# Optimization experiments

Hardware: AMD Instinct MI355X
Metric: run time of the kernel (lower is better)

The kernel has to match this reference:

```python
import jax, jax.numpy as jnp
import numpy as np

ANCESTOR_INDEX = [[], [0], [0], [0], [0, 1], [0, 2], [0, 3], [0, 1, 4], [0, 2, 5], [0, 3, 6], [0, 1, 4, 7], [0, 2, 5, 8], [0, 3, 6, 9], [0, 3, 6, 9], [0, 3, 6, 9], [0, 3, 6, 9, 12], [0, 3, 6, 9, 13], [0, 3, 6, 9, 14], [0, 3, 6, 9, 13, 16], [0, 3, 6, 9, 14, 17], [0, 3, 6, 9, 13, 16, 18], [0, 3, 6, 9, 14, 17, 19], [0, 3, 6, 9, 13, 16, 18, 20], [0, 3, 6, 9, 14, 17, 19, 21]]
HID = 1024
NP6 = 6
MAXIN = HID + NP6 * 8 + 6


def setup_inputs() -> dict:
    key = jax.random.key(0)
    ks = jax.random.split(key, 18)
    B, T = 2048, 16
    s = 0.02
    inp = {
        'x': jax.random.normal(ks[0], (B, T, 256), jnp.float32),
        'init_pose': jax.random.normal(ks[1], (B, T, 144), jnp.float32) * 0.1,
        'init_shape': jax.random.normal(ks[2], (B, T, 10), jnp.float32) * 0.1,
        'init_cam': jax.random.normal(ks[3], (B, T, 3), jnp.float32) * 0.1,
        'fc1_w': jax.random.normal(ks[4], (HID, 256 + 10), jnp.float32) * s,
        'fc1_b': jnp.zeros((HID,), jnp.float32),
        'fc2_w': jax.random.normal(ks[5], (HID, 256 + 144), jnp.float32) * s,
        'fc2_b': jnp.zeros((HID,), jnp.float32),
        'decshape_w': jax.random.normal(ks[6], (10, HID), jnp.float32) * s,
        'decshape_b': jnp.zeros((10,), jnp.float32),
        'deccam_w': jax.random.normal(ks[7], (3, 2 * HID + 3), jnp.float32) * s,
        'deccam_b': jnp.zeros((3,), jnp.float32),
        'ktd_w': jax.random.normal(ks[8], (24, NP6, MAXIN), jnp.float32) * 0.01,
        'ktd_b': jnp.zeros((24, NP6), jnp.float32),
    }
    return inp


def reference(x, init_pose, init_shape, init_cam, fc1_w, fc1_b, fc2_w, fc2_b,
              decshape_w, decshape_b, deccam_w, deccam_b, ktd_w, ktd_b):
    # fc1 / fc2 (dropout is identity in eval mode)
    xc_shape_cam = jnp.concatenate([x, init_shape], -1) @ fc1_w.T + fc1_b   # [B,T,HID]
    xc_pose_cam = jnp.concatenate([x, init_pose], -1) @ fc2_w.T + fc2_b     # [B,T,HID]

    pose = []
    for j, anc in enumerate(ANCESTOR_INDEX):
        parts = [xc_pose_cam] + [pose[i] for i in anc] + [init_pose[..., j:j + 6]]
        inp = jnp.concatenate(parts, -1)
        pad = MAXIN - inp.shape[-1]
        if pad:
            inp = jnp.pad(inp, ((0, 0), (0, 0), (0, pad)))
        pose.append(jnp.einsum('btd,od->bto', inp, ktd_w[j]) + ktd_b[j])
    pred_pose = jnp.concatenate(pose, -1) + init_pose                        # [B,T,144]

    pred_shape = xc_shape_cam @ decshape_w.T + decshape_b + init_shape      # [B,T,10]
    pred_cam = (jnp.concatenate([xc_pose_cam, xc_shape_cam, init_cam], -1)
                @ deccam_w.T + deccam_b + init_cam)                          # [B,T,3]

    pred_pose = pred_pose.reshape(-1, 144)
    pred_shape = pred_shape.reshape(-1, 10)
    pred_cam = pred_cam.reshape(-1, 3)
    # theta layout matches original output: [cam | pose | shape]
    return jnp.concatenate([pred_cam, pred_pose, pred_shape], -1)           # [B*T,157]
```

## Files before the change

kernel.cpp:

```cpp
#include <hip/hip_runtime.h>
#include <hip/hip_bf16.h>

typedef __attribute__((ext_vector_type(8))) short bf16x8;
typedef __attribute__((ext_vector_type(4))) float f32x4;

static constexpr int ALEN[24] = {0,1,1,1,2,2,2,3,3,3,4,4,4,4,4,5,5,5,6,6,7,7,8,8};
static constexpr int AOFF[24] = {0,0,1,2,3,5,7,9,12,15,18,22,26,30,34,38,43,48,53,59,65,72,79,87};
static constexpr int AFLAT[95] = {
  0, 0, 0,
  0,1, 0,2, 0,3,
  0,1,4, 0,2,5, 0,3,6,
  0,1,4,7, 0,2,5,8, 0,3,6,9, 0,3,6,9, 0,3,6,9,
  0,3,6,9,12, 0,3,6,9,13, 0,3,6,9,14,
  0,3,6,9,13,16, 0,3,6,9,14,17,
  0,3,6,9,13,16,18, 0,3,6,9,14,17,19,
  0,3,6,9,13,16,18,20, 0,3,6,9,14,17,19,21};
static constexpr int LVLN[9] = {1,3,3,3,5,3,2,2,2};
static constexpr int LVLJ[9][5] = {
  {0,0,0,0,0},{1,2,3,0,0},{4,5,6,0,0},{7,8,9,0,0},{10,11,12,13,14},
  {15,16,17,0,0},{18,19,0,0,0},{20,21,0,0,0},{22,23,0,0,0}};

static __device__ __forceinline__ unsigned short f2bf(float f) {
  unsigned int u = __float_as_uint(f);
  u = (u + 0x7fffu + ((u >> 16) & 1u)) >> 16;
  return (unsigned short)u;
}

static __device__ __forceinline__ bf16x8 pack8(float4 lo, float4 hi) {
  bf16x8 r;
  r[0] = (short)f2bf(lo.x); r[1] = (short)f2bf(lo.y);
  r[2] = (short)f2bf(lo.z); r[3] = (short)f2bf(lo.w);
  r[4] = (short)f2bf(hi.x); r[5] = (short)f2bf(hi.y);
  r[6] = (short)f2bf(hi.z); r[7] = (short)f2bf(hi.w);
  return r;
}

__global__ __launch_bounds__(256) void combine_plus(const float* __restrict__ ktd,
                                                    const float* __restrict__ dcw,
                                                    const float* __restrict__ dsw,
                                                    const float* __restrict__ w2,
                                                    const float* __restrict__ b2,
                                                    const float* __restrict__ w1,
                                                    const float* __restrict__ b1,
                                                    float* __restrict__ Gp,
                                                    float* __restrict__ Hp,
                                                    float* __restrict__ S) {
  __shared__ float shpool[5760];
  const int tid = threadIdx.x;

  if (blockIdx.y == 41) {
    if (blockIdx.x >= 4 || blockIdx.z != 0) return;
    float* Sl = shpool;
    const int c0 = blockIdx.x * 36;
    for (int lv = 0; lv < 9; lv++) {
      int units = LVLN[lv] * 54;
      for (int u = tid; u < units; u += 256) {
        int jj = u / 54, rem = u % 54, r = rem / 9, q = rem % 9;
        int j = LVLJ[lv][jj];
        int t = 6 * j + r;
        int cb = c0 + q * 4;
        f32x4 v;
        v[0] = (t == cb)     ? 1.f : 0.f;
        v[1] = (t == cb + 1) ? 1.f : 0.f;
        v[2] = (t == cb + 2) ? 1.f : 0.f;
        v[3] = (t == cb + 3) ? 1.f : 0.f;
        const float* wrow = ktd + (size_t)t * 1078 + 1024;
        for (int a = 0; a < ALEN[j]; a++) {
          int anc = AFLAT[AOFF[j] + a];
          const float* w = wrow + 6 * a;
          #pragma unroll
          for (int k = 0; k < 6; k++) {
            f32x4 s4 = *(const f32x4*)&Sl[(anc * 6 + k) * 40 + q * 4];
            float wk = w[k];
            v[0] += wk * s4[0]; v[1] += wk * s4[1];
            v[2] += wk * s4[2]; v[3] += wk * s4[3];
          }
        }
        *(f32x4*)&Sl[t * 40 + q * 4] = v;
      }
      __syncthreads();
    }
    for (int i = tid; i < 144 * 36; i += 256) {
      int t = i / 36, cc = i % 36;
      S[t * 144 + c0 + cc] = Sl[t * 40 + cc];
    }
    return;
  }

  const bool isH = blockIdx.y >= 37;
  if (isH && blockIdx.x >= 5) return;
  float (*red)[4][64] = (float(*)[4][64])shpool;
  const int w = tid >> 6, lane = tid & 63;
  const int c = blockIdx.x * 64 + lane;
  const int h0 = blockIdx.z * 128 + w * 32;

  const float* vp[4];
  int o0;
  if (!isH) {
    o0 = blockIdx.y * 4;
    #pragma unroll
    for (int oi = 0; oi < 4; oi++) {
      int o = o0 + oi; if (o > 146) o = 146;
      vp[oi] = (o < 144) ? (ktd + (size_t)o * 1078) : (dcw + (size_t)(o - 144) * 2051);
    }
  } else {
    o0 = (blockIdx.y - 37) * 4;
    #pragma unroll
    for (int oi = 0; oi < 4; oi++) {
      int o = o0 + oi; if (o > 12) o = 12;
      vp[oi] = (o < 10) ? (dsw + (size_t)o * 1024) : (dcw + (size_t)(o - 10) * 2051 + 1024);
    }
  }

  float acc[4] = {0.f, 0.f, 0.f, 0.f};
  if (!isH) {
    #pragma unroll 16
    for (int hh = 0; hh < 32; hh++) {
      int h = h0 + hh;
      float wv = (c < 400) ? w2[h * 400 + c] : ((c == 400) ? b2[h] : 0.f);
      #pragma unroll
      for (int oi = 0; oi < 4; oi++) acc[oi] += vp[oi][h] * wv;
    }
  } else {
    #pragma unroll 16
    for (int hh = 0; hh < 32; hh++) {
      int h = h0 + hh;
      float wv = (c < 266) ? w1[h * 266 + c] : ((c == 266) ? b1[h] : 0.f);
      #pragma unroll
      for (int oi = 0; oi < 4; oi++) acc[oi] += vp[oi][h] * wv;
    }
  }

  #pragma unroll
  for (int oi = 0; oi < 4; oi++) red[w][oi][lane] = acc[oi];
  __syncthreads();
  if (w == 0) {
    #pragma unroll
    for (int oi = 0; oi < 4; oi++) {
      int o = o0 + oi;
      float s = red[0][oi][lane] + red[1][oi][lane] + red[2][oi][lane] + red[3][oi][lane];
      if (!isH) {
        if (o < 147 && c <= 400) Gp[(size_t)blockIdx.z * 59200 + o * 401 + c] = s;
      } else {
        if (o < 13 && c <= 266) Hp[(size_t)blockIdx.z * 3520 + o * 267 + c] = s;
      }
    }
  }
}

static __device__ __forceinline__ float gsum(const float* __restrict__ Gp, int t, int c) {
  float s = 0.f;
  #pragma unroll
  for (int z = 0; z < 8; z++) s += Gp[(size_t)z * 59200 + t * 401 + c];
  return s;
}
static __device__ __forceinline__ float hsum(const float* __restrict__ Hp, int t, int c) {
  float s = 0.f;
  #pragma unroll
  for (int z = 0; z < 8; z++) s += Hp[(size_t)z * 3520 + t * 267 + c];
  return s;
}

__global__ __launch_bounds__(256) void assembleM(const float* __restrict__ Gp,
                                                 const float* __restrict__ Hp,
                                                 const float* __restrict__ dcw,
                                                 const float* __restrict__ dcb,
                                                 const float* __restrict__ dsb,
                                                 const float* __restrict__ ktd,
                                                 const float* __restrict__ ktdb,
                                                 float* __restrict__ M0,
                                                 float* __restrict__ C0) {
  int o = blockIdx.x;
  for (int c = threadIdx.x; c < 424; c += 256) {
    float val = 0.f;
    if (c < 413) {
      if (o < 3) {
        if (c < 400) val += gsum(Gp, 144 + o, c);
        if (c < 256) val += hsum(Hp, 10 + o, c);
        if (c >= 400 && c < 410) val += hsum(Hp, 10 + o, 256 + (c - 400));
        if (c >= 410) {
          val += dcw[(size_t)o * 2051 + 2048 + (c - 410)];
          if ((c - 410) == o) val += 1.f;
        }
      } else if (o < 147) {
        int t = o - 3, j = t / 6;
        if (c < 400) val = gsum(Gp, t, c);
        int cj = c - 256 - j;
        if (cj >= 0 && cj < 6) val += ktd[(size_t)t * 1078 + 1024 + 6 * ALEN[j] + cj];
      } else if (o < 157) {
        int s = o - 147;
        if (c < 256) val = hsum(Hp, s, c);
        if (c >= 400 && c < 410) {
          val += hsum(Hp, s, 256 + (c - 400));
          if ((c - 400) == s) val += 1.f;
        }
      }
    }
    M0[o * 424 + c] = val;
  }
  if (threadIdx.x == 0 && o < 157) {
    float bv;
    if (o < 3)        bv = gsum(Gp, 144 + o, 400) + hsum(Hp, 10 + o, 266) + dcb[o];
    else if (o < 147) bv = gsum(Gp, o - 3, 400) + ktdb[o - 3];
    else              bv = hsum(Hp, o - 147, 266) + dsb[o - 147];
    C0[o] = bv;
  }
}

__global__ __launch_bounds__(256) void foldS(const float* __restrict__ S,
                                             const float* __restrict__ M0,
                                             const float* __restrict__ C0,
                                             unsigned short* __restrict__ Mb,
                                             float* __restrict__ Cb) {
  int o = blockIdx.x;
  int c = blockIdx.y * 212 + threadIdx.x;
  bool act = (threadIdx.x < 212) && (c < 424);
  if (o < 3 || o >= 147) {
    if (act) Mb[o * 424 + c] = f2bf(M0[o * 424 + c]);
    if (threadIdx.x == 0 && blockIdx.y == 0) Cb[o] = (o < 157) ? C0[o] : 0.f;
    return;
  }
  int t = o - 3;
  __shared__ float Sl[144];
  if (threadIdx.x < 144) Sl[threadIdx.x] = S[t * 144 + threadIdx.x];
  __syncthreads();
  if (act) {
    float acc = 0.f;
    #pragma unroll 16
    for (int k = 0; k < 144; k++) acc += Sl[k] * M0[(3 + k) * 424 + c];
    if (c == 256 + t) acc += 1.f;
    Mb[o * 424 + c] = f2bf(acc);
  }
  if (threadIdx.x == 0 && blockIdx.y == 0) {
    float acc = 0.f;
    for (int k = 0; k < 144; k++) acc += Sl[k] * C0[3 + k];
    Cb[o] = acc;
  }
}

__global__ __launch_bounds__(512, 4) void main_gemm(const float* __restrict__ x,
                                                    const float* __restrict__ ipose,
                                                    const float* __restrict__ ishape,
                                                    const float* __restrict__ icam,
                                                    const unsigned short* __restrict__ Mb,
                                                    const float* __restrict__ Cb,
                                                    float* __restrict__ out) {
  __shared__ alignas(16) unsigned short Bl[80 * 424];
  const int tid = threadIdx.x;
  const int w = tid >> 6, lane = tid & 63;
  const int m = lane & 15, g = lane >> 4;
  const int h = blockIdx.y;
  const int rowbase = blockIdx.x * 128 + w * 16;
  const int row = rowbase + m;
  const float* xr = x + (size_t)row * 256;
  const float* pr = ipose + (size_t)row * 144;

  {
    const bf16x8* src = (const bf16x8*)(Mb + (size_t)h * 80 * 424);
    bf16x8* dst = (bf16x8*)Bl;
    for (int i = tid; i < 80 * 424 / 8; i += 512) dst[i] = src[i];
  }

  bf16x8 areg[13];
  {
    float4 lo[5], hi[5];
    #pragma unroll
    for (int k = 0; k < 5; k++) {
      const float* p = xr + k * 32 + g * 8;
      lo[k] = *(const float4*)p; hi[k] = *(const float4*)(p + 4);
    }
    #pragma unroll
    for (int k = 0; k < 5; k++) {
      asm volatile("" :: "v"(lo[k].x), "v"(lo[k].y), "v"(lo[k].z), "v"(lo[k].w));
      asm volatile("" :: "v"(hi[k].x), "v"(hi[k].y), "v"(hi[k].z), "v"(hi[k].w));
    }
    #pragma unroll
    for (int k = 0; k < 5; k++) areg[k] = pack8(lo[k], hi[k]);
  }
  {
    float4 lo[4], hi[4];
    #pragma unroll
    for (int k = 0; k < 3; k++) {
      const float* p = xr + (k + 5) * 32 + g * 8;
      lo[k] = *(const float4*)p; hi[k] = *(const float4*)(p + 4);
    }
    {
      const float* p = pr + g * 8;
      lo[3] = *(const float4*)p; hi[3] = *(const float4*)(p + 4);
    }
    #pragma unroll
    for (int k = 0; k < 4; k++) {
      asm volatile("" :: "v"(lo[k].x), "v"(lo[k].y), "v"(lo[k].z), "v"(lo[k].w));
      asm volatile("" :: "v"(hi[k].x), "v"(hi[k].y), "v"(hi[k].z), "v"(hi[k].w));
    }
    #pragma unroll
    for (int k = 0; k < 4; k++) areg[k + 5] = pack8(lo[k], hi[k]);
  }
  {
    float4 lo[4], hi[4];
    #pragma unroll
    for (int k = 0; k < 3; k++) {
      const float* p = pr + (k + 1) * 32 + g * 8;
      lo[k] = *(const float4*)p; hi[k] = *(const float4*)(p + 4);
    }
    if (g < 2) {
      const float* p = pr + 128 + g * 8;
      lo[3] = *(const float4*)p; hi[3] = *(const float4*)(p + 4);
    } else if (g == 2) {
      const float* p = ishape + (size_t)row * 10;
      lo[3] = make_float4(p[0], p[1], p[2], p[3]);
      hi[3] = make_float4(p[4], p[5], p[6], p[7]);
    } else {
      const float* p = ishape + (size_t)row * 10;
      const float* q = icam + (size_t)row * 3;
      lo[3] = make_float4(p[8], p[9], q[0], q[1]);
      hi[3] = make_float4(q[2], 0.f, 0.f, 0.f);
    }
    #pragma unroll
    for (int k = 0; k < 4; k++) {
      asm volatile("" :: "v"(lo[k].x), "v"(lo[k].y), "v"(lo[k].z), "v"(lo[k].w));
      asm volatile("" :: "v"(hi[k].x), "v"(hi[k].y), "v"(hi[k].z), "v"(hi[k].w));
    }
    #pragma unroll
    for (int k = 0; k < 4; k++) areg[k + 9] = pack8(lo[k], hi[k]);
  }

  __syncthreads();

  f32x4 acc[5];
  #pragma unroll
  for (int n = 0; n < 5; n++) acc[n] = (f32x4){0.f, 0.f, 0.f, 0.f};

  #pragma unroll
  for (int k = 0; k < 13; k++) {
    #pragma unroll
    for (int n = 0; n < 5; n++) {
      bf16x8 b = *(const bf16x8*)&Bl[(n * 16 + m) * 424 + k * 32 + g * 8];
      acc[n] = __builtin_amdgcn_mfma_f32_16x16x32_bf16(areg[k], b, acc[n], 0, 0, 0);
    }
  }

  #pragma unroll
  for (int n = 0; n < 5; n++) {
    int col = h * 80 + n * 16 + m;
    if (col < 157) {
      float bias = Cb[col];
      #pragma unroll
      for (int q = 0; q < 4; q++)
        out[(size_t)(rowbase + g * 4 + q) * 157 + col] = acc[n][q] + bias;
    }
  }
}

extern "C" void kernel_launch(void* const* d_in, const int* in_sizes, int n_in,
                              void* d_out, int out_size, void* d_ws, size_t ws_size,
                              hipStream_t stream) {
  const float* x      = (const float*)d_in[0];
  const float* ipose  = (const float*)d_in[1];
  const float* ishape = (const float*)d_in[2];
  const float* icam   = (const float*)d_in[3];
  const float* fc1w   = (const float*)d_in[4];
  const float* fc1b   = (const float*)d_in[5];
  const float* fc2w   = (const float*)d_in[6];
  const float* fc2b   = (const float*)d_in[7];
  const float* dsw    = (const float*)d_in[8];
  const float* dsb    = (const float*)d_in[9];
  const float* dcw    = (const float*)d_in[10];
  const float* dcb    = (const float*)d_in[11];
  const float* ktd    = (const float*)d_in[12];
  const float* ktdb   = (const float*)d_in[13];
  int rows = in_sizes[0] / 256;
  float* ws = (float*)d_ws;

  float* Gp = ws;
  float* Hp = ws + 473600;
  float* M0 = ws + 501760;
  float* C0 = ws + 569600;
  float* S  = ws + 569760;
  float* Cb = ws + 590496;
  unsigned short* Mb = (unsigned short*)(ws + 590656);

  combine_plus<<<dim3(7, 42, 8), 256, 0, stream>>>(ktd, dcw, dsw, fc2w, fc2b,
                                                   fc1w, fc1b, Gp, Hp, S);
  assembleM<<<160, 256, 0, stream>>>(Gp, Hp, dcw, dcb, dsb, ktd, ktdb, M0, C0);
  foldS<<<dim3(160, 2), 256, 0, stream>>>(S, M0, C0, Mb, Cb);
  main_gemm<<<dim3(rows / 128, 2), 512, 0, stream>>>(x, ipose, ishape, icam,
                                                     Mb, Cb, (float*)d_out);
}
```

Measured before the change: 61.85 us.

## Fuse setup kernels into one persistent kernel with software grid barriers

Merges the weight-combine, matrix-assembly and S-fold kernels into a single persistent 256-block kernel that loops over the former work units and separates phases with atomic-counter grid barriers. The aim is to remove kernel launch gaps between the small preprocessing stages. It adds a memset for the counters and spin-wait barriers, and relies on all 256 blocks being co-resident to avoid deadlock.

```diff
diff --git a/kernel.cpp b/kernel.cpp
--- a/kernel.cpp
+++ b/kernel.cpp
@@ -35,119 +35,6 @@
   return r;
 }
 
-__global__ __launch_bounds__(256) void combine_plus(const float* __restrict__ ktd,
-                                                    const float* __restrict__ dcw,
-                                                    const float* __restrict__ dsw,
-                                                    const float* __restrict__ w2,
-                                                    const float* __restrict__ b2,
-                                                    const float* __restrict__ w1,
-                                                    const float* __restrict__ b1,
-                                                    float* __restrict__ Gp,
-                                                    float* __restrict__ Hp,
-                                                    float* __restrict__ S) {
-  __shared__ float shpool[5760];
-  const int tid = threadIdx.x;
-
-  if (blockIdx.y == 41) {
-    if (blockIdx.x >= 4 || blockIdx.z != 0) return;
-    float* Sl = shpool;
-    const int c0 = blockIdx.x * 36;
-    for (int lv = 0; lv < 9; lv++) {
-      int units = LVLN[lv] * 54;
-      for (int u = tid; u < units; u += 256) {
-        int jj = u / 54, rem = u % 54, r = rem / 9, q = rem % 9;
-        int j = LVLJ[lv][jj];
-        int t = 6 * j + r;
-        int cb = c0 + q * 4;
-        f32x4 v;
-        v[0] = (t == cb)     ? 1.f : 0.f;
-        v[1] = (t == cb + 1) ? 1.f : 0.f;
-        v[2] = (t == cb + 2) ? 1.f : 0.f;
-        v[3] = (t == cb + 3) ? 1.f : 0.f;
-        const float* wrow = ktd + (size_t)t * 1078 + 1024;
-        for (int a = 0; a < ALEN[j]; a++) {
-          int anc = AFLAT[AOFF[j] + a];
-          const float* w = wrow + 6 * a;
-          #pragma unroll
-          for (int k = 0; k < 6; k++) {
-            f32x4 s4 = *(const f32x4*)&Sl[(anc * 6 + k) * 40 + q * 4];
-            float wk = w[k];
-            v[0] += wk * s4[0]; v[1] += wk * s4[1];
-            v[2] += wk * s4[2]; v[3] += wk * s4[3];
-          }
-        }
-        *(f32x4*)&Sl[t * 40 + q * 4] = v;
-      }
-      __syncthreads();
-    }
-    for (int i = tid; i < 144 * 36; i += 256) {
-      int t = i / 36, cc = i % 36;
-      S[t * 144 + c0 + cc] = Sl[t * 40 + cc];
-    }
-    return;
-  }
-
-  const bool isH = blockIdx.y >= 37;
-  if (isH && blockIdx.x >= 5) return;
-  float (*red)[4][64] = (float(*)[4][64])shpool;
-  const int w = tid >> 6, lane = tid & 63;
-  const int c = blockIdx.x * 64 + lane;
-  const int h0 = blockIdx.z * 128 + w * 32;
-
-  const float* vp[4];
-  int o0;
-  if (!isH) {
-    o0 = blockIdx.y * 4;
-    #pragma unroll
-    for (int oi = 0; oi < 4; oi++) {
-      int o = o0 + oi; if (o > 146) o = 146;
-      vp[oi] = (o < 144) ? (ktd + (size_t)o * 1078) : (dcw + (size_t)(o - 144) * 2051);
-    }
-  } else {
-    o0 = (blockIdx.y - 37) * 4;
-    #pragma unroll
-    for (int oi = 0; oi < 4; oi++) {
-      int o = o0 + oi; if (o > 12) o = 12;
-      vp[oi] = (o < 10) ? (dsw + (size_t)o * 1024) : (dcw + (size_t)(o - 10) * 2051 + 1024);
-    }
-  }
-
-  float acc[4] = {0.f, 0.f, 0.f, 0.f};
-  if (!isH) {
-    #pragma unroll 16
-    for (int hh = 0; hh < 32; hh++) {
-      int h = h0 + hh;
-      float wv = (c < 400) ? w2[h * 400 + c] : ((c == 400) ? b2[h] : 0.f);
-      #pragma unroll
-      for (int oi = 0; oi < 4; oi++) acc[oi] += vp[oi][h] * wv;
-    }
-  } else {
-    #pragma unroll 16
-    for (int hh = 0; hh < 32; hh++) {
-      int h = h0 + hh;
-      float wv = (c < 266) ? w1[h * 266 + c] : ((c == 266) ? b1[h] : 0.f);
-      #pragma unroll
-      for (int oi = 0; oi < 4; oi++) acc[oi] += vp[oi][h] * wv;
-    }
-  }
-
-  #pragma unroll
-  for (int oi = 0; oi < 4; oi++) red[w][oi][lane] = acc[oi];
-  __syncthreads();
-  if (w == 0) {
-    #pragma unroll
-    for (int oi = 0; oi < 4; oi++) {
-      int o = o0 + oi;
-      float s = red[0][oi][lane] + red[1][oi][lane] + red[2][oi][lane] + red[3][oi][lane];
-      if (!isH) {
-        if (o < 147 && c <= 400) Gp[(size_t)blockIdx.z * 59200 + o * 401 + c] = s;
-      } else {
-        if (o < 13 && c <= 266) Hp[(size_t)blockIdx.z * 3520 + o * 267 + c] = s;
-      }
-    }
-  }
-}
-
 static __device__ __forceinline__ float gsum(const float* __restrict__ Gp, int t, int c) {
   float s = 0.f;
   #pragma unroll
@@ -161,80 +48,208 @@
   return s;
 }
 
-__global__ __launch_bounds__(256) void assembleM(const float* __restrict__ Gp,
-                                                 const float* __restrict__ Hp,
+static __device__ __forceinline__ void grid_sync(unsigned int* cnt) {
+  __syncthreads();
+  __threadfence();
+  if (threadIdx.x == 0) {
+    atomicAdd(cnt, 1u);
+    while (atomicAdd(cnt, 0u) < 256u) __builtin_amdgcn_s_sleep(8);
+  }
+  __syncthreads();
+  __threadfence();
+}
+
+__global__ __launch_bounds__(256) void setup_all(const float* __restrict__ ktd,
                                                  const float* __restrict__ dcw,
+                                                 const float* __restrict__ dsw,
+                                                 const float* __restrict__ w2,
+                                                 const float* __restrict__ b2,
+                                                 const float* __restrict__ w1,
+                                                 const float* __restrict__ b1,
                                                  const float* __restrict__ dcb,
                                                  const float* __restrict__ dsb,
-                                                 const float* __restrict__ ktd,
                                                  const float* __restrict__ ktdb,
+                                                 float* __restrict__ Gp,
+                                                 float* __restrict__ Hp,
+                                                 float* __restrict__ S,
                                                  float* __restrict__ M0,
-                                                 float* __restrict__ C0) {
-  int o = blockIdx.x;
-  for (int c = threadIdx.x; c < 424; c += 256) {
-    float val = 0.f;
-    if (c < 413) {
-      if (o < 3) {
-        if (c < 400) val += gsum(Gp, 144 + o, c);
-        if (c < 256) val += hsum(Hp, 10 + o, c);
-        if (c >= 400 && c < 410) val += hsum(Hp, 10 + o, 256 + (c - 400));
-        if (c >= 410) {
-          val += dcw[(size_t)o * 2051 + 2048 + (c - 410)];
-          if ((c - 410) == o) val += 1.f;
+                                                 float* __restrict__ C0,
+                                                 unsigned short* __restrict__ Mb,
+                                                 float* __restrict__ Cb,
+                                                 unsigned int* __restrict__ syncc) {
+  __shared__ float shpool[5760];
+  const int tid = threadIdx.x;
+  const int w = tid >> 6, lane = tid & 63;
+
+  for (unsigned u = blockIdx.x; u < 2236; u += 256) {
+    __syncthreads();
+    if (u < 2072) {
+      int ux = u % 7, uy = (u / 7) % 37, uz = u / 259;
+      int c = ux * 64 + lane, h0 = uz * 128 + w * 32;
+      float (*red)[4][64] = (float(*)[4][64])shpool;
+      const float* vp[4];
+      int o0 = uy * 4;
+      #pragma unroll
+      for (int oi = 0; oi < 4; oi++) {
+        int o = o0 + oi; if (o > 146) o = 146;
+        vp[oi] = (o < 144) ? (ktd + (size_t)o * 1078) : (dcw + (size_t)(o - 144) * 2051);
+      }
+      float acc[4] = {0.f, 0.f, 0.f, 0.f};
+      #pragma unroll 16
+      for (int hh = 0; hh < 32; hh++) {
+        int h = h0 + hh;
+        float wv = (c < 400) ? w2[h * 400 + c] : ((c == 400) ? b2[h] : 0.f);
+        #pragma unroll
+        for (int oi = 0; oi < 4; oi++) acc[oi] += vp[oi][h] * wv;
+      }
+      #pragma unroll
+      for (int oi = 0; oi < 4; oi++) red[w][oi][lane] = acc[oi];
+      __syncthreads();
+      if (w == 0) {
+        #pragma unroll
+        for (int oi = 0; oi < 4; oi++) {
+          int o = o0 + oi;
+          float s = red[0][oi][lane] + red[1][oi][lane] + red[2][oi][lane] + red[3][oi][lane];
+          if (o < 147 && c <= 400) Gp[(size_t)uz * 59200 + o * 401 + c] = s;
         }
-      } else if (o < 147) {
-        int t = o - 3, j = t / 6;
-        if (c < 400) val = gsum(Gp, t, c);
-        int cj = c - 256 - j;
-        if (cj >= 0 && cj < 6) val += ktd[(size_t)t * 1078 + 1024 + 6 * ALEN[j] + cj];
-      } else if (o < 157) {
-        int s = o - 147;
-        if (c < 256) val = hsum(Hp, s, c);
-        if (c >= 400 && c < 410) {
-          val += hsum(Hp, s, 256 + (c - 400));
-          if ((c - 400) == s) val += 1.f;
+      }
+    } else if (u < 2232) {
+      int v = u - 2072;
+      int ux = v % 5, uy = (v / 5) % 4, uz = v / 20;
+      int c = ux * 64 + lane, h0 = uz * 128 + w * 32;
+      float (*red)[4][64] = (float(*)[4][64])shpool;
+      const float* vp[4];
+      int o0 = uy * 4;
+      #pragma unroll
+      for (int oi = 0; oi < 4; oi++) {
+        int o = o0 + oi; if (o > 12) o = 12;
+        vp[oi] = (o < 10) ? (dsw + (size_t)o * 1024) : (dcw + (size_t)(o - 10) * 2051 + 1024);
+      }
+      float acc[4] = {0.f, 0.f, 0.f, 0.f};
+      #pragma unroll 16
+      for (int hh = 0; hh < 32; hh++) {
+        int h = h0 + hh;
+        float wv = (c < 266) ? w1[h * 266 + c] : ((c == 266) ? b1[h] : 0.f);
+        #pragma unroll
+        for (int oi = 0; oi < 4; oi++) acc[oi] += vp[oi][h] * wv;
+      }
+      #pragma unroll
+      for (int oi = 0; oi < 4; oi++) red[w][oi][lane] = acc[oi];
+      __syncthreads();
+      if (w == 0) {
+        #pragma unroll
+        for (int oi = 0; oi < 4; oi++) {
+          int o = o0 + oi;
+          float s = red[0][oi][lane] + red[1][oi][lane] + red[2][oi][lane] + red[3][oi][lane];
+          if (o < 13 && c <= 266) Hp[(size_t)uz * 3520 + o * 267 + c] = s;
         }
       }
-    }
-    M0[o * 424 + c] = val;
-  }
-  if (threadIdx.x == 0 && o < 157) {
-    float bv;
-    if (o < 3)        bv = gsum(Gp, 144 + o, 400) + hsum(Hp, 10 + o, 266) + dcb[o];
-    else if (o < 147) bv = gsum(Gp, o - 3, 400) + ktdb[o - 3];
-    else              bv = hsum(Hp, o - 147, 266) + dsb[o - 147];
-    C0[o] = bv;
-  }
-}
-
-__global__ __launch_bounds__(256) void foldS(const float* __restrict__ S,
-                                             const float* __restrict__ M0,
-                                             const float* __restrict__ C0,
-                                             unsigned short* __restrict__ Mb,
-                                             float* __restrict__ Cb) {
-  int o = blockIdx.x;
-  int c = blockIdx.y * 212 + threadIdx.x;
-  bool act = (threadIdx.x < 212) && (c < 424);
-  if (o < 3 || o >= 147) {
-    if (act) Mb[o * 424 + c] = f2bf(M0[o * 424 + c]);
-    if (threadIdx.x == 0 && blockIdx.y == 0) Cb[o] = (o < 157) ? C0[o] : 0.f;
-    return;
-  }
-  int t = o - 3;
-  __shared__ float Sl[144];
-  if (threadIdx.x < 144) Sl[threadIdx.x] = S[t * 144 + threadIdx.x];
-  __syncthreads();
-  if (act) {
-    float acc = 0.f;
-    #pragma unroll 16
-    for (int k = 0; k < 144; k++) acc += Sl[k] * M0[(3 + k) * 424 + c];
-    if (c == 256 + t) acc += 1.f;
-    Mb[o * 424 + c] = f2bf(acc);
-  }
-  if (threadIdx.x == 0 && blockIdx.y == 0) {
-    float acc = 0.f;
-    for (int k = 0; k < 144; k++) acc += Sl[k] * C0[3 + k];
-    Cb[o] = acc;
+    } else {
+      float* Sl = shpool;
+      const int c0 = (u - 2232) * 36;
+      for (int lv = 0; lv < 9; lv++) {
+        int units = LVLN[lv] * 54;
+        for (int uu = tid; uu < units; uu += 256) {
+          int jj = uu / 54, rem = uu % 54, r = rem / 9, q = rem % 9;
+          int j = LVLJ[lv][jj];
+          int t = 6 * j + r;
+          int cb = c0 + q * 4;
+          f32x4 v;
+          v[0] = (t == cb)     ? 1.f : 0.f;
+          v[1] = (t == cb + 1) ? 1.f : 0.f;
+          v[2] = (t == cb + 2) ? 1.f : 0.f;
+          v[3] = (t == cb + 3) ? 1.f : 0.f;
+          const float* wrow = ktd + (size_t)t * 1078 + 1024;
+          for (int a = 0; a < ALEN[j]; a++) {
+            int anc = AFLAT[AOFF[j] + a];
+            const float* wp = wrow + 6 * a;
+            #pragma unroll
+            for (int k = 0; k < 6; k++) {
+              f32x4 s4 = *(const f32x4*)&Sl[(anc * 6 + k) * 40 + q * 4];
+              float wk = wp[k];
+              v[0] += wk * s4[0]; v[1] += wk * s4[1];
+              v[2] += wk * s4[2]; v[3] += wk * s4[3];
+            }
+          }
+          *(f32x4*)&Sl[t * 40 + q * 4] = v;
+        }
+        __syncthreads();
+      }
+      for (int i = tid; i < 144 * 36; i += 256) {
+        int t = i / 36, cc = i % 36;
+        S[t * 144 + c0 + cc] = Sl[t * 40 + cc];
+      }
+    }
+  }
+
+  grid_sync(syncc);
+
+  if (blockIdx.x < 160) {
+    int o = blockIdx.x;
+    for (int c = tid; c < 424; c += 256) {
+      float val = 0.f;
+      if (c < 413) {
+        if (o < 3) {
+          if (c < 400) val += gsum(Gp, 144 + o, c);
+          if (c < 256) val += hsum(Hp, 10 + o, c);
+          if (c >= 400 && c < 410) val += hsum(Hp, 10 + o, 256 + (c - 400));
+          if (c >= 410) {
+            val += dcw[(size_t)o * 2051 + 2048 + (c - 410)];
+            if ((c - 410) == o) val += 1.f;
+          }
+        } else if (o < 147) {
+          int t = o - 3, j = t / 6;
+          if (c < 400) val = gsum(Gp, t, c);
+          int cj = c - 256 - j;
+          if (cj >= 0 && cj < 6) val += ktd[(size_t)t * 1078 + 1024 + 6 * ALEN[j] + cj];
+        } else if (o < 157) {
+          int s = o - 147;
+          if (c < 256) val = hsum(Hp, s, c);
+          if (c >= 400 && c < 410) {
+            val += hsum(Hp, s, 256 + (c - 400));
+            if ((c - 400) == s) val += 1.f;
+          }
+        }
+      }
+      M0[o * 424 + c] = val;
+    }
+    if (tid == 0 && o < 157) {
+      float bv;
+      if (o < 3)        bv = gsum(Gp, 144 + o, 400) + hsum(Hp, 10 + o, 266) + dcb[o];
+      else if (o < 147) bv = gsum(Gp, o - 3, 400) + ktdb[o - 3];
+      else              bv = hsum(Hp, o - 147, 266) + dsb[o - 147];
+      C0[o] = bv;
+    }
+  }
+
+  grid_sync(syncc + 1);
+
+  for (unsigned u = blockIdx.x; u < 320; u += 256) {
+    int o = u % 160, cy = u / 160;
+    int c = cy * 212 + tid;
+    bool act = (tid < 212) && (c < 424);
+    __syncthreads();
+    if (o < 3 || o >= 147) {
+      if (act) Mb[o * 424 + c] = f2bf(M0[o * 424 + c]);
+      if (tid == 0 && cy == 0) Cb[o] = (o < 157) ? C0[o] : 0.f;
+    } else {
+      int t = o - 3;
+      float* Sl = shpool;
+      if (tid < 144) Sl[tid] = S[t * 144 + tid];
+      __syncthreads();
+      if (act) {
+        float acc = 0.f;
+        #pragma unroll 16
+        for (int k = 0; k < 144; k++) acc += Sl[k] * M0[(3 + k) * 424 + c];
+        if (c == 256 + t) acc += 1.f;
+        Mb[o * 424 + c] = f2bf(acc);
+      }
+      if (tid == 0 && cy == 0) {
+        float acc = 0.f;
+        for (int k = 0; k < 144; k++) acc += Sl[k] * C0[3 + k];
+        Cb[o] = acc;
+      }
+    }
   }
 }
 
@@ -379,11 +394,12 @@
   float* S  = ws + 569760;
   float* Cb = ws + 590496;
   unsigned short* Mb = (unsigned short*)(ws + 590656);
-
-  combine_plus<<<dim3(7, 42, 8), 256, 0, stream>>>(ktd, dcw, dsw, fc2w, fc2b,
-                                                   fc1w, fc1b, Gp, Hp, S);
-  assembleM<<<160, 256, 0, stream>>>(Gp, Hp, dcw, dcb, dsb, ktd, ktdb, M0, C0);
-  foldS<<<dim3(160, 2), 256, 0, stream>>>(S, M0, C0, Mb, Cb);
+  unsigned int* syncc = (unsigned int*)(ws + 624576);
+
+  hipMemsetAsync(syncc, 0, 8, stream);
+  setup_all<<<256, 256, 0, stream>>>(ktd, dcw, dsw, fc2w, fc2b, fc1w, fc1b,
+                                     dcb, dsb, ktdb, Gp, Hp, S, M0, C0,
+                                     Mb, Cb, syncc);
   main_gemm<<<dim3(rows / 128, 2), 512, 0, stream>>>(x, ipose, ishape, icam,
                                                      Mb, Cb, (float*)d_out);
 }
```

Measured after the change: 164.1 us. +165.3%, slower.
